# Optimization experiments

Hardware: AMD Instinct MI355X
Metric: run time of the kernel (lower is better)

Reference implementation:

```python
import jax, jax.numpy as jnp
import numpy as np

TEMPERATURE = 0.07
BASE_TEMPERATURE = 0.07


def setup_inputs() -> dict:
    key = jax.random.key(0)
    k1, k2 = jax.random.split(key)
    feat1 = jax.random.normal(k1, (4096, 128), dtype=jnp.float32)
    feat2 = jax.random.normal(k2, (4096, 128), dtype=jnp.float32)
    return {"feat1": feat1, "feat2": feat2}


def reference(feat1, feat2):
    # world_size = 1 -> gather is identity; N = per-gpu batch size
    N = feat1.shape[0]
    two_n = 2 * N
    features = jnp.concatenate([feat1, feat2], axis=0)          # [2N, C]
    # F.normalize(dim=1)
    norm = jnp.linalg.norm(features, axis=1, keepdims=True)
    features = features / jnp.maximum(norm, 1e-12)
    logits = jnp.matmul(features, features.T) / TEMPERATURE      # [2N, 2N]
    logits = logits - jax.lax.stop_gradient(
        jnp.max(logits, axis=1, keepdims=True))
    # neg_mask = ~eye: sum of exp over off-diagonal entries per row
    exp_sum = jnp.sum(jnp.exp(logits), axis=1) - jnp.exp(jnp.diagonal(logits))
    # pos_mask: row i pairs with column (i + N) mod 2N
    idx = jnp.arange(two_n)
    pos = logits[idx, (idx + N) % two_n]                          # [2N]
    log_prob = pos - jnp.log(exp_sum)
    loss = -(TEMPERATURE / BASE_TEMPERATURE) * jnp.mean(log_prob)
    return loss
```

## Files before the change

kernel.cpp:

```cpp
#include <hip/hip_runtime.h>

typedef unsigned short u16;
typedef __attribute__((ext_vector_type(8))) short short8;
typedef __attribute__((ext_vector_type(4))) float f32x4;

#define INVT 14.285714285714286f

__device__ __forceinline__ u16 f2bf(float f) {
  union { float f; unsigned u; } v; v.f = f;
  unsigned u = v.u;
  u += 0x7fffu + ((u >> 16) & 1u);
  return (u16)(u >> 16);
}
__device__ __forceinline__ float bf2f(u16 h) {
  union { unsigned u; float f; } v; v.u = ((unsigned)h) << 16;
  return v.f;
}

__global__ void norm_kernel(const float* __restrict__ f1, const float* __restrict__ f2,
                            u16* __restrict__ F, float* __restrict__ dvec,
                            float* __restrict__ pos, float* __restrict__ E, int N) {
  int i = blockIdx.x;
  int l = threadIdx.x;
  if (l < 2) E[2 * i + l] = 0.0f;
  const float* a = f1 + (size_t)i * 128;
  const float* b = f2 + (size_t)i * 128;
  float a0 = a[l], a1 = a[l + 64];
  float b0 = b[l], b1 = b[l + 64];
  float sa = a0 * a0 + a1 * a1;
  float sb = b0 * b0 + b1 * b1;
#pragma unroll
  for (int o = 32; o; o >>= 1) { sa += __shfl_xor(sa, o); sb += __shfl_xor(sb, o); }
  float ia = 1.0f / fmaxf(sqrtf(sa), 1e-12f);
  float ib = 1.0f / fmaxf(sqrtf(sb), 1e-12f);
  u16 ba0 = f2bf(a0 * ia), ba1 = f2bf(a1 * ia);
  u16 bb0 = f2bf(b0 * ib), bb1 = f2bf(b1 * ib);
  u16* Fa = F + (size_t)i * 128;
  u16* Fb = F + (size_t)(i + N) * 128;
  Fa[l] = ba0; Fa[l + 64] = ba1;
  Fb[l] = bb0; Fb[l + 64] = bb1;
  float fa0 = bf2f(ba0), fa1 = bf2f(ba1);
  float fb0 = bf2f(bb0), fb1 = bf2f(bb1);
  float s1 = fa0 * fa0 + fa1 * fa1;
  float s2 = fb0 * fb0 + fb1 * fb1;
  float cr = fa0 * fb0 + fa1 * fb1;
#pragma unroll
  for (int o = 32; o; o >>= 1) {
    s1 += __shfl_xor(s1, o); s2 += __shfl_xor(s2, o); cr += __shfl_xor(cr, o);
  }
  if (l == 0) {
    dvec[i]     = __expf((s1 - 1.0f) * INVT);
    dvec[i + N] = __expf((s2 - 1.0f) * INVT);
    pos[i] = cr;
    pos[i + N] = cr;
  }
}

__device__ __forceinline__ void glds16(const u16* g, u16* l) {
  __builtin_amdgcn_global_load_lds((const __attribute__((address_space(1))) void*)g,
                                   (__attribute__((address_space(3))) void*)l,
                                   16, 0, 0);
}

__global__ __launch_bounds__(256, 2) void gemm_exp_kernel(const u16* __restrict__ F,
                                                          float* __restrict__ E) {
  __shared__ __align__(16) u16 At[128 * 128];
  __shared__ __align__(16) u16 Bt[128 * 128];
  __shared__ float colsum[128];
  __shared__ float rowsum[128];
  const int tid = threadIdx.x;
  const int wave = tid >> 6, lane = tid & 63;
  int p = blockIdx.x;
  int r = (int)((sqrtf(8.0f * (float)p + 1.0f) - 1.0f) * 0.5f);
  while ((r + 1) * (r + 2) / 2 <= p) ++r;
  while (r * (r + 1) / 2 > p) --r;
  const int bj = r, bi = p - r * (r + 1) / 2;
  const u16* Ab = F + (size_t)bi * (128 * 128);
  const u16* Bb = F + (size_t)bj * (128 * 128);
  if (tid < 128) { colsum[tid] = 0.0f; rowsum[tid] = 0.0f; }
#pragma unroll
  for (int t = 0; t < 8; ++t) {
    int chunk = wave * 8 + t;
    int g = chunk * 64 + lane;
    int gg = g ^ ((g >> 4) & 7);
    glds16(Ab + (size_t)gg * 8, &At[chunk * 512]);
    glds16(Bb + (size_t)gg * 8, &Bt[chunk * 512]);
  }
  __syncthreads();

  const int wr = wave >> 1, wc = wave & 1;
  const int q = lane >> 4, m = lane & 15;
  f32x4 acc[4][4];
#pragma unroll
  for (int fr = 0; fr < 4; ++fr)
#pragma unroll
    for (int cf = 0; cf < 4; ++cf) acc[fr][cf] = (f32x4)(0.0f);

#pragma unroll
  for (int ks = 0; ks < 4; ++ks) {
    const int c = ks * 4 + q;
    short8 av[4], bv[4];
#pragma unroll
    for (int fr = 0; fr < 4; ++fr) {
      int rr = wr * 64 + fr * 16 + m;
      av[fr] = *(const short8*)&At[rr * 128 + ((c ^ (rr & 7)) * 8)];
    }
#pragma unroll
    for (int cf = 0; cf < 4; ++cf) {
      int rr = wc * 64 + cf * 16 + m;
      bv[cf] = *(const short8*)&Bt[rr * 128 + ((c ^ (rr & 7)) * 8)];
    }
#pragma unroll
    for (int fr = 0; fr < 4; ++fr)
#pragma unroll
      for (int cf = 0; cf < 4; ++cf)
        acc[fr][cf] = __builtin_amdgcn_mfma_f32_16x16x32_bf16(av[fr], bv[cf], acc[fr][cf], 0, 0, 0);
  }

  float cs[4] = {0.f, 0.f, 0.f, 0.f};
  float rs[16];
#pragma unroll
  for (int i = 0; i < 16; ++i) rs[i] = 0.f;
#pragma unroll
  for (int cf = 0; cf < 4; ++cf)
#pragma unroll
    for (int fr = 0; fr < 4; ++fr)
#pragma unroll
      for (int rg = 0; rg < 4; ++rg) {
        float e = __expf((acc[fr][cf][rg] - 1.0f) * INVT);
        cs[cf] += e;
        rs[fr * 4 + rg] += e;
      }
#pragma unroll
  for (int cf = 0; cf < 4; ++cf) {
    cs[cf] += __shfl_xor(cs[cf], 16);
    cs[cf] += __shfl_xor(cs[cf], 32);
    if (q == 0) atomicAdd(&colsum[wc * 64 + cf * 16 + m], cs[cf]);
  }
  if (bi != bj) {
#pragma unroll
    for (int i = 0; i < 16; ++i) {
#pragma unroll
      for (int o = 1; o < 16; o <<= 1) rs[i] += __shfl_xor(rs[i], o);
    }
    if (m == 0) {
#pragma unroll
      for (int i = 0; i < 16; ++i)
        atomicAdd(&rowsum[wr * 64 + (i >> 2) * 16 + q * 4 + (i & 3)], rs[i]);
    }
  }
  __syncthreads();
  if (tid < 128) {
    atomicAdd(&E[bj * 128 + tid], colsum[tid]);
    if (bi != bj) atomicAdd(&E[bi * 128 + tid], rowsum[tid]);
  }
}

__global__ void finish_kernel(const float* __restrict__ E, const float* __restrict__ dvec,
                              const float* __restrict__ pos, float* __restrict__ out,
                              int TWO_N, float scale) {
  float t = 0.0f;
  for (int i = threadIdx.x; i < TWO_N; i += 1024)
    t += (pos[i] - 1.0f) * INVT - logf(E[i] - dvec[i]);
#pragma unroll
  for (int o = 32; o; o >>= 1) t += __shfl_xor(t, o);
  __shared__ float wsum[16];
  int wave = threadIdx.x >> 6, lane = threadIdx.x & 63;
  if (lane == 0) wsum[wave] = t;
  __syncthreads();
  if (threadIdx.x == 0) {
    float s = 0.0f;
#pragma unroll
    for (int k = 0; k < 16; ++k) s += wsum[k];
    out[0] = s * scale;
  }
}

extern "C" void kernel_launch(void* const* d_in, const int* in_sizes, int n_in,
                              void* d_out, int out_size, void* d_ws, size_t ws_size,
                              hipStream_t stream) {
  const float* f1 = (const float*)d_in[0];
  const float* f2 = (const float*)d_in[1];
  const int N = in_sizes[0] / 128;
  const int TWO_N = 2 * N;
  const int NB = TWO_N / 128;
  const int NTILES = NB * (NB + 1) / 2;

  char* ws = (char*)d_ws;
  u16*   F    = (u16*)ws;
  float* dvec = (float*)(ws + (size_t)TWO_N * 128 * 2);
  float* pos  = dvec + TWO_N;
  float* E    = pos + TWO_N;

  norm_kernel<<<N, 64, 0, stream>>>(f1, f2, F, dvec, pos, E, N);
  gemm_exp_kernel<<<NTILES, 256, 0, stream>>>(F, E);
  finish_kernel<<<1, 1024, 0, stream>>>(E, dvec, pos, (float*)d_out, TWO_N,
                                        -1.0f / (float)TWO_N);
}
```

Baseline: 89.41 us.

## Split K into two halves with staged waits, 512-thread blocks, exp2 and DPP reductions

The GEMM kernel now runs 8 waves per block, with each wave owning a 32x64 sub-tile. Shared memory is split into two K-halves so compute on the first half can start while the second half is still loading, using manual s_waitcnt vmcnt barriers. The exp is rewritten as a native exp2 with a folded FMA constant. Row-sum reductions use DPP row_ror adds instead of shuffles. The risks are the hand-coded waitcnt counts and more wave-level atomics into shared memory.

```diff
diff --git a/kernel.cpp b/kernel.cpp
--- a/kernel.cpp
+++ b/kernel.cpp
@@ -5,6 +5,7 @@
 typedef __attribute__((ext_vector_type(4))) float f32x4;
 
 #define INVT 14.285714285714286f
+#define EXP2C 20.609640474436812f
 
 __device__ __forceinline__ u16 f2bf(float f) {
   union { float f; unsigned u; } v; v.f = f;
@@ -15,6 +16,14 @@
 __device__ __forceinline__ float bf2f(u16 h) {
   union { unsigned u; float f; } v; v.u = ((unsigned)h) << 16;
   return v.f;
+}
+
+__device__ __forceinline__ float fast_exp2(float x) {
+#if __has_builtin(__builtin_amdgcn_exp2f)
+  return __builtin_amdgcn_exp2f(x);
+#else
+  return exp2f(x);
+#endif
 }
 
 __global__ void norm_kernel(const float* __restrict__ f1, const float* __restrict__ f2,
@@ -49,8 +58,8 @@
     s1 += __shfl_xor(s1, o); s2 += __shfl_xor(s2, o); cr += __shfl_xor(cr, o);
   }
   if (l == 0) {
-    dvec[i]     = __expf((s1 - 1.0f) * INVT);
-    dvec[i + N] = __expf((s2 - 1.0f) * INVT);
+    dvec[i]     = fast_exp2(fmaf(s1, EXP2C, -EXP2C));
+    dvec[i + N] = fast_exp2(fmaf(s2, EXP2C, -EXP2C));
     pos[i] = cr;
     pos[i + N] = cr;
   }
@@ -62,10 +71,16 @@
                                    16, 0, 0);
 }
 
-__global__ __launch_bounds__(256, 2) void gemm_exp_kernel(const u16* __restrict__ F,
+template <int CTRL>
+__device__ __forceinline__ float ror_add(float x) {
+  int r = __builtin_amdgcn_update_dpp(0, __float_as_int(x), CTRL, 0xF, 0xF, false);
+  return x + __int_as_float(r);
+}
+
+__global__ __launch_bounds__(512, 4) void gemm_exp_kernel(const u16* __restrict__ F,
                                                           float* __restrict__ E) {
-  __shared__ __align__(16) u16 At[128 * 128];
-  __shared__ __align__(16) u16 Bt[128 * 128];
+  __shared__ __align__(16) u16 At[2][128][64];
+  __shared__ __align__(16) u16 Bt[2][128][64];
   __shared__ float colsum[128];
   __shared__ float rowsum[128];
   const int tid = threadIdx.x;
@@ -75,59 +90,70 @@
   while ((r + 1) * (r + 2) / 2 <= p) ++r;
   while (r * (r + 1) / 2 > p) --r;
   const int bj = r, bi = p - r * (r + 1) / 2;
-  const u16* Ab = F + (size_t)bi * (128 * 128);
-  const u16* Bb = F + (size_t)bj * (128 * 128);
+  const u16* __restrict__ Ab = F + (size_t)bi * (128 * 128);
+  const u16* __restrict__ Bb = F + (size_t)bj * (128 * 128);
   if (tid < 128) { colsum[tid] = 0.0f; rowsum[tid] = 0.0f; }
-#pragma unroll
-  for (int t = 0; t < 8; ++t) {
-    int chunk = wave * 8 + t;
-    int g = chunk * 64 + lane;
-    int gg = g ^ ((g >> 4) & 7);
-    glds16(Ab + (size_t)gg * 8, &At[chunk * 512]);
-    glds16(Bb + (size_t)gg * 8, &Bt[chunk * 512]);
-  }
-  __syncthreads();
+
+  const int lrow = lane >> 3, lcol = lane & 7;
+#pragma unroll
+  for (int h = 0; h < 2; ++h)
+#pragma unroll
+    for (int t = 0; t < 2; ++t) {
+      const int row = wave * 16 + t * 8 + lrow;
+      const size_t gsrc = (size_t)(row * 16 + h * 8 + (lcol ^ (row & 7))) * 8;
+      u16* da = (u16*)At + h * 8192 + (wave * 2 + t) * 512;
+      u16* db = (u16*)Bt + h * 8192 + (wave * 2 + t) * 512;
+      glds16(Ab + gsrc, da);
+      glds16(Bb + gsrc, db);
+    }
 
   const int wr = wave >> 1, wc = wave & 1;
   const int q = lane >> 4, m = lane & 15;
-  f32x4 acc[4][4];
-#pragma unroll
-  for (int fr = 0; fr < 4; ++fr)
+  f32x4 acc[2][4];
+#pragma unroll
+  for (int fr = 0; fr < 2; ++fr)
 #pragma unroll
     for (int cf = 0; cf < 4; ++cf) acc[fr][cf] = (f32x4)(0.0f);
 
-#pragma unroll
-  for (int ks = 0; ks < 4; ++ks) {
-    const int c = ks * 4 + q;
-    short8 av[4], bv[4];
-#pragma unroll
-    for (int fr = 0; fr < 4; ++fr) {
-      int rr = wr * 64 + fr * 16 + m;
-      av[fr] = *(const short8*)&At[rr * 128 + ((c ^ (rr & 7)) * 8)];
+  auto kstep = [&](int ks) {
+    const int h = ks >> 1;
+    const int c = (ks & 1) * 4 + q;
+    const u16* Ah = (const u16*)At + h * 8192;
+    const u16* Bh = (const u16*)Bt + h * 8192;
+    short8 av[2], bv[4];
+#pragma unroll
+    for (int fr = 0; fr < 2; ++fr) {
+      int rr = wr * 32 + fr * 16 + m;
+      av[fr] = *(const short8*)&Ah[rr * 64 + ((c ^ (rr & 7)) * 8)];
     }
 #pragma unroll
     for (int cf = 0; cf < 4; ++cf) {
       int rr = wc * 64 + cf * 16 + m;
-      bv[cf] = *(const short8*)&Bt[rr * 128 + ((c ^ (rr & 7)) * 8)];
-    }
-#pragma unroll
-    for (int fr = 0; fr < 4; ++fr)
+      bv[cf] = *(const short8*)&Bh[rr * 64 + ((c ^ (rr & 7)) * 8)];
+    }
+#pragma unroll
+    for (int fr = 0; fr < 2; ++fr)
 #pragma unroll
       for (int cf = 0; cf < 4; ++cf)
         acc[fr][cf] = __builtin_amdgcn_mfma_f32_16x16x32_bf16(av[fr], bv[cf], acc[fr][cf], 0, 0, 0);
-  }
+  };
+
+  asm volatile("s_waitcnt vmcnt(4) lgkmcnt(0)\n\ts_barrier" ::: "memory");
+  kstep(0);
+  kstep(1);
+  asm volatile("s_waitcnt vmcnt(0)\n\ts_barrier" ::: "memory");
+  kstep(2);
+  kstep(3);
 
   float cs[4] = {0.f, 0.f, 0.f, 0.f};
-  float rs[16];
-#pragma unroll
-  for (int i = 0; i < 16; ++i) rs[i] = 0.f;
+  float rs[8] = {0.f, 0.f, 0.f, 0.f, 0.f, 0.f, 0.f, 0.f};
 #pragma unroll
   for (int cf = 0; cf < 4; ++cf)
 #pragma unroll
-    for (int fr = 0; fr < 4; ++fr)
+    for (int fr = 0; fr < 2; ++fr)
 #pragma unroll
       for (int rg = 0; rg < 4; ++rg) {
-        float e = __expf((acc[fr][cf][rg] - 1.0f) * INVT);
+        float e = fast_exp2(fmaf(acc[fr][cf][rg], EXP2C, -EXP2C));
         cs[cf] += e;
         rs[fr * 4 + rg] += e;
       }
@@ -139,14 +165,13 @@
   }
   if (bi != bj) {
 #pragma unroll
-    for (int i = 0; i < 16; ++i) {
-#pragma unroll
-      for (int o = 1; o < 16; o <<= 1) rs[i] += __shfl_xor(rs[i], o);
-    }
-    if (m == 0) {
-#pragma unroll
-      for (int i = 0; i < 16; ++i)
-        atomicAdd(&rowsum[wr * 64 + (i >> 2) * 16 + q * 4 + (i & 3)], rs[i]);
+    for (int i = 0; i < 8; ++i) {
+      float v = rs[i];
+      v = ror_add<0x121>(v);
+      v = ror_add<0x122>(v);
+      v = ror_add<0x124>(v);
+      v = ror_add<0x128>(v);
+      if (m == i) atomicAdd(&rowsum[wr * 32 + (i >> 2) * 16 + q * 4 + (i & 3)], v);
     }
   }
   __syncthreads();
@@ -193,7 +218,7 @@
   float* E    = pos + TWO_N;
 
   norm_kernel<<<N, 64, 0, stream>>>(f1, f2, F, dvec, pos, E, N);
-  gemm_exp_kernel<<<NTILES, 256, 0, stream>>>(F, E);
+  gemm_exp_kernel<<<NTILES, 512, 0, stream>>>(F, E);
   finish_kernel<<<1, 1024, 0, stream>>>(E, dvec, pos, (float*)d_out, TWO_N,
                                         -1.0f / (float)TWO_N);
 }
```

Result: faster. 83.95 us (-6.1%).
